# Kernel tuning notes

Measured on AMD Instinct MI355X. Metric: run time of the kernel, lower is better.

Reference implementation:

```python
import jax, jax.numpy as jnp
import numpy as np

B_SZ, L, D = 8, 8192, 256


def setup_inputs() -> dict:
    key = jax.random.key(0)
    kx, ka, kb, kc = jax.random.split(key, 4)
    x = jax.random.normal(kx, (B_SZ, L, D), dtype=jnp.float32)
    # Scale A so its spectral radius is < 1; otherwise the 8192-step linear
    # recurrence overflows. (Random Gaussian DxD with std s has norm ~ 2*s*sqrt(D).)
    A = jax.random.normal(ka, (D, D), dtype=jnp.float32) * (0.4 / np.sqrt(D))
    B = jax.random.normal(kb, (D, D), dtype=jnp.float32) * 0.05
    C = jax.random.normal(kc, (D, D), dtype=jnp.float32) * 0.05
    return {"x": x, "A": A, "B": B, "C": C}


def reference(x, A, B, C):
    # state_t = state_{t-1} @ A + x_t @ B.T ; out_t = state_t @ C.T
    # Dropout is identity in eval mode and omitted.
    b = x.shape[0]
    h = A.shape[0]
    init = jnp.zeros((b, h), dtype=x.dtype)
    Bt = B.T  # (input_dim, hidden_dim) -> math uses x @ B.T per source
    Ct = C.T

    def step(state, xt):  # xt: (b, d)
        state = state @ A + xt @ Bt
        return state, state @ Ct

    _, ys = jax.lax.scan(step, init, jnp.swapaxes(x, 0, 1))  # ys: (l, b, out)
    return jnp.swapaxes(ys, 0, 1)  # (b, l, out)
```

## Files before the change

kernel.cpp:

```cpp
#include <hip/hip_runtime.h>

#define BSZ 8
#define LSEQ 8192
#define DDIM 256
#define CHUNK 16
#define WARM 32
#define STEPS (CHUNK + WARM)
#define CPB 16

typedef float f32x4 __attribute__((ext_vector_type(4)));
typedef _Float16 h8 __attribute__((ext_vector_type(8)));
typedef _Float16 h4 __attribute__((ext_vector_type(4)));
typedef _Float16 h2 __attribute__((ext_vector_type(2)));


__global__ __launch_bounds__(256) void k_gemm_u(
    const float* __restrict__ x, const float* __restrict__ A,
    const float* __restrict__ B, const float* __restrict__ C,
    _Float16* __restrict__ U, _Float16* __restrict__ AhT,
    _Float16* __restrict__ Ch, _Float16* __restrict__ Zph) {
  __shared__ __align__(16) _Float16 xh[64][264];
  __shared__ __align__(16) _Float16 bs[64][264];
  const int tid = threadIdx.x, wv = tid >> 6, lane = tid & 63;
  const int l15 = lane & 15, q = lane >> 4;

  if (blockIdx.x < 256) {
    const int r = blockIdx.x;
    AhT[tid * 256 + r] = (_Float16)A[r * 256 + tid];
    Ch[r * 256 + tid] = (_Float16)C[r * 256 + tid];
    if (r == 0) { Zph[tid] = (_Float16)0.f; Zph[tid + 256] = (_Float16)0.f; }
  }

  const size_t rowbase = (size_t)blockIdx.x * 64;
#pragma unroll 4
  for (int i = 0; i < 16; ++i) {
    const int f4 = i * 256 + tid;
    const int row = f4 >> 6, c4 = f4 & 63;
    float4 v = *(const float4*)(x + (rowbase + row) * 256 + c4 * 4);
    h4 h;
    h[0] = (_Float16)v.x; h[1] = (_Float16)v.y; h[2] = (_Float16)v.z; h[3] = (_Float16)v.w;
    *(h4*)&xh[row][c4 * 4] = h;
  }

#pragma unroll 1
  for (int cbk = 0; cbk < 4; ++cbk) {
    __syncthreads();
#pragma unroll 4
    for (int i = 0; i < 16; ++i) {
      const int f4 = i * 256 + tid;
      const int row = f4 >> 6, c4 = f4 & 63;
      float4 v = *(const float4*)(B + (size_t)(cbk * 64 + row) * 256 + c4 * 4);
      h4 h;
      h[0] = (_Float16)v.x; h[1] = (_Float16)v.y; h[2] = (_Float16)v.z; h[3] = (_Float16)v.w;
      *(h4*)&bs[row][c4 * 4] = h;
    }
    __syncthreads();

    f32x4 acc[4] = {};
#pragma unroll
    for (int kb = 0; kb < 8; ++kb) {
      h8 af = *(const h8*)&xh[wv * 16 + l15][kb * 32 + q * 8];
#pragma unroll
      for (int ct = 0; ct < 4; ++ct) {
        h8 bf = *(const h8*)&bs[ct * 16 + l15][kb * 32 + q * 8];
        acc[ct] = __builtin_amdgcn_mfma_f32_16x16x32_f16(af, bf, acc[ct], 0, 0, 0);
      }
    }
    const size_t grow = rowbase + wv * 16 + q * 4;
#pragma unroll
    for (int r = 0; r < 4; ++r) {
      h4 hv;
      hv[0] = (_Float16)acc[0][r]; hv[1] = (_Float16)acc[1][r];
      hv[2] = (_Float16)acc[2][r]; hv[3] = (_Float16)acc[3][r];
      *(h4*)(U + (grow + r) * 256 + cbk * 64 + l15 * 4) = hv;
    }
  }
}

__global__ __launch_bounds__(512, 2) void k_scan(const _Float16* __restrict__ U,
                                                 const _Float16* __restrict__ AhT,
                                                 const _Float16* __restrict__ Ch,
                                                 const _Float16* __restrict__ Zp,
                                                 float* __restrict__ O) {
  __shared__ __align__(16) _Float16 st[2][CPB][264];
  const int tid = threadIdx.x, wv = tid >> 6, lane = tid & 63;
  const int l15 = lane & 15, q = lane >> 4;
  const int g64 = wv >> 1, hf = wv & 1;
  const int b = blockIdx.x >> 5;
  const int c0 = (blockIdx.x & 31) * CPB;
  const size_t bbase = (size_t)b * LSEQ;

  h8 bf[2][8], cf[2][8];
#pragma unroll
  for (int ctl = 0; ctl < 2; ++ctl)
#pragma unroll
    for (int kb = 0; kb < 8; ++kb) {
      const size_t mo = (size_t)(g64 * 64 + (2 * hf + ctl) * 16 + l15) * 256 + kb * 32 + q * 8;
      bf[ctl][kb] = *(const h8*)(AhT + mo);
      cf[ctl][kb] = *(const h8*)(Ch + mo);
    }

  for (int i = tid; i < CPB * 264; i += 512) ((_Float16*)st[0])[i] = (_Float16)0.f;

  auto uload = [&](int t, int r) -> h2 {
    const int lr = (c0 + q * 4 + r) * CHUNK + t;
    const _Float16* p = (lr < 0 || lr >= LSEQ)
                            ? (Zp + l15 * 4 + 2 * hf)
                            : (U + (bbase + (size_t)lr) * 256 + g64 * 64 + l15 * 4 + 2 * hf);
    return *(const h2*)p;
  };

  float* op[4];
#pragma unroll
  for (int r = 0; r < 4; ++r)
    op[r] = O + (bbase + (size_t)(c0 + q * 4 + r) * CHUNK) * 256 + g64 * 64 + 2 * hf * 16 + l15;

  h2 up0 = uload(-WARM, 0), up1 = uload(-WARM, 1), up2 = uload(-WARM, 2), up3 = uload(-WARM, 3);
  __syncthreads();

  int cb = 0;
#pragma unroll 1
  for (int g = 0; g <= STEPS; ++g) {
    const int t = g - WARM;
    h2 un0 = uload(t + 1, 0), un1 = uload(t + 1, 1), un2 = uload(t + 1, 2), un3 = uload(t + 1, 3);
    if (g < STEPS) {
      f32x4 acc[2];
#pragma unroll
      for (int ctl = 0; ctl < 2; ++ctl) {
        acc[ctl][0] = (float)up0[ctl]; acc[ctl][1] = (float)up1[ctl];
        acc[ctl][2] = (float)up2[ctl]; acc[ctl][3] = (float)up3[ctl];
      }
      if (t >= 1) {
        f32x4 acc2[2] = {};
#pragma unroll
        for (int kb = 0; kb < 8; ++kb) {
          h8 af = *(const h8*)&st[cb][l15][kb * 32 + q * 8];
#pragma unroll
          for (int ctl = 0; ctl < 2; ++ctl)
            acc[ctl] = __builtin_amdgcn_mfma_f32_16x16x32_f16(af, bf[ctl][kb], acc[ctl], 0, 0, 0);
#pragma unroll
          for (int ctl = 0; ctl < 2; ++ctl)
            acc2[ctl] = __builtin_amdgcn_mfma_f32_16x16x32_f16(af, cf[ctl][kb], acc2[ctl], 0, 0, 0);
        }
#pragma unroll
        for (int ctl = 0; ctl < 2; ++ctl)
#pragma unroll
          for (int r = 0; r < 4; ++r)
            st[cb ^ 1][q * 4 + r][g64 * 64 + (2 * hf + ctl) * 16 + l15] = (_Float16)acc[ctl][r];
#pragma unroll
        for (int r = 0; r < 4; ++r) {
          op[r][0] = acc2[0][r];
          op[r][16] = acc2[1][r];
          op[r] += 256;
        }
      } else {
#pragma unroll
        for (int kb = 0; kb < 8; ++kb) {
          h8 af = *(const h8*)&st[cb][l15][kb * 32 + q * 8];
#pragma unroll
          for (int ctl = 0; ctl < 2; ++ctl)
            acc[ctl] = __builtin_amdgcn_mfma_f32_16x16x32_f16(af, bf[ctl][kb], acc[ctl], 0, 0, 0);
        }
#pragma unroll
        for (int ctl = 0; ctl < 2; ++ctl)
#pragma unroll
          for (int r = 0; r < 4; ++r)
            st[cb ^ 1][q * 4 + r][g64 * 64 + (2 * hf + ctl) * 16 + l15] = (_Float16)acc[ctl][r];
      }
    } else {
      f32x4 acc2[2] = {};
#pragma unroll
      for (int kb = 0; kb < 8; ++kb) {
        h8 af = *(const h8*)&st[cb][l15][kb * 32 + q * 8];
#pragma unroll
        for (int ctl = 0; ctl < 2; ++ctl)
          acc2[ctl] = __builtin_amdgcn_mfma_f32_16x16x32_f16(af, cf[ctl][kb], acc2[ctl], 0, 0, 0);
      }
#pragma unroll
      for (int r = 0; r < 4; ++r) {
        op[r][0] = acc2[0][r];
        op[r][16] = acc2[1][r];
      }
    }
    asm volatile("s_waitcnt lgkmcnt(0)" ::: "memory");
    __builtin_amdgcn_s_barrier();
    asm volatile("" ::: "memory");
    up0 = un0; up1 = un1; up2 = un2; up3 = un3;
    cb ^= 1;
  }
}

extern "C" void kernel_launch(void* const* d_in, const int* in_sizes, int n_in,
                              void* d_out, int out_size, void* d_ws, size_t ws_size,
                              hipStream_t stream) {
  const float* x = (const float*)d_in[0];
  const float* A = (const float*)d_in[1];
  const float* B = (const float*)d_in[2];
  const float* C = (const float*)d_in[3];

  char* ws = (char*)d_ws;
  _Float16* U = (_Float16*)ws;
  _Float16* AhT = (_Float16*)(ws + 33554432);
  _Float16* Ch = (_Float16*)(ws + 33554432 + 131072);
  _Float16* Zph = (_Float16*)(ws + 33554432 + 262144);
  float* out = (float*)d_out;

  hipLaunchKernelGGL(k_gemm_u, dim3(1024), dim3(256), 0, stream, x, A, B, C, U, AhT,
                     Ch, Zph);
  hipLaunchKernelGGL(k_scan, dim3(256), dim3(512), 0, stream, U, AhT, Ch, Zph, out);
}
```

Baseline: 178.0 us.

## Load B fragments directly into registers and halve rows per GEMM block

The U = x·Bᵀ GEMM kernel no longer stages B through shared memory in four column chunks with barriers. Each wave now reads its 64 output columns of B straight from global memory into registers, converting to fp16 on the way, and reuses them across two 16-row tiles. Blocks cover 32 rows instead of 64 and the grid doubles, which cuts LDS use and barriers. The cost is that every block rereads all of B from global or L2 memory, and there is less reuse per block.

```diff
diff --git a/kernel.cpp b/kernel.cpp
--- a/kernel.cpp
+++ b/kernel.cpp
@@ -19,8 +19,7 @@
     const float* __restrict__ B, const float* __restrict__ C,
     _Float16* __restrict__ U, _Float16* __restrict__ AhT,
     _Float16* __restrict__ Ch, _Float16* __restrict__ Zph) {
-  __shared__ __align__(16) _Float16 xh[64][264];
-  __shared__ __align__(16) _Float16 bs[64][264];
+  __shared__ __align__(16) _Float16 xh[32][264];
   const int tid = threadIdx.x, wv = tid >> 6, lane = tid & 63;
   const int l15 = lane & 15, q = lane >> 4;
 
@@ -31,9 +30,9 @@
     if (r == 0) { Zph[tid] = (_Float16)0.f; Zph[tid + 256] = (_Float16)0.f; }
   }
 
-  const size_t rowbase = (size_t)blockIdx.x * 64;
-#pragma unroll 4
-  for (int i = 0; i < 16; ++i) {
+  const size_t rowbase = (size_t)blockIdx.x * 32;
+#pragma unroll
+  for (int i = 0; i < 8; ++i) {
     const int f4 = i * 256 + tid;
     const int row = f4 >> 6, c4 = f4 & 63;
     float4 v = *(const float4*)(x + (rowbase + row) * 256 + c4 * 4);
@@ -41,38 +40,39 @@
     h[0] = (_Float16)v.x; h[1] = (_Float16)v.y; h[2] = (_Float16)v.z; h[3] = (_Float16)v.w;
     *(h4*)&xh[row][c4 * 4] = h;
   }
-
-#pragma unroll 1
-  for (int cbk = 0; cbk < 4; ++cbk) {
-    __syncthreads();
-#pragma unroll 4
-    for (int i = 0; i < 16; ++i) {
-      const int f4 = i * 256 + tid;
-      const int row = f4 >> 6, c4 = f4 & 63;
-      float4 v = *(const float4*)(B + (size_t)(cbk * 64 + row) * 256 + c4 * 4);
-      h4 h;
-      h[0] = (_Float16)v.x; h[1] = (_Float16)v.y; h[2] = (_Float16)v.z; h[3] = (_Float16)v.w;
-      *(h4*)&bs[row][c4 * 4] = h;
-    }
-    __syncthreads();
-
-    f32x4 acc[4] = {};
+  __syncthreads();
+
+  f32x4 acc[2][4] = {};
+#pragma unroll
+  for (int ct = 0; ct < 4; ++ct) {
+    const int n = wv * 64 + ct * 16 + l15;
+    h8 bf[8];
 #pragma unroll
     for (int kb = 0; kb < 8; ++kb) {
-      h8 af = *(const h8*)&xh[wv * 16 + l15][kb * 32 + q * 8];
-#pragma unroll
-      for (int ct = 0; ct < 4; ++ct) {
-        h8 bf = *(const h8*)&bs[ct * 16 + l15][kb * 32 + q * 8];
-        acc[ct] = __builtin_amdgcn_mfma_f32_16x16x32_f16(af, bf, acc[ct], 0, 0, 0);
-      }
-    }
-    const size_t grow = rowbase + wv * 16 + q * 4;
+      const float* bp = B + (size_t)n * 256 + kb * 32 + q * 8;
+      float4 b0 = *(const float4*)bp, b1 = *(const float4*)(bp + 4);
+      h8 f;
+      f[0] = (_Float16)b0.x; f[1] = (_Float16)b0.y; f[2] = (_Float16)b0.z; f[3] = (_Float16)b0.w;
+      f[4] = (_Float16)b1.x; f[5] = (_Float16)b1.y; f[6] = (_Float16)b1.z; f[7] = (_Float16)b1.w;
+      bf[kb] = f;
+    }
+#pragma unroll
+    for (int rt = 0; rt < 2; ++rt)
+#pragma unroll
+      for (int kb = 0; kb < 8; ++kb) {
+        h8 af = *(const h8*)&xh[rt * 16 + l15][kb * 32 + q * 8];
+        acc[rt][ct] = __builtin_amdgcn_mfma_f32_16x16x32_f16(af, bf[kb], acc[rt][ct], 0, 0, 0);
+      }
+  }
+#pragma unroll
+  for (int rt = 0; rt < 2; ++rt) {
+    const size_t grow = rowbase + rt * 16 + q * 4;
 #pragma unroll
     for (int r = 0; r < 4; ++r) {
       h4 hv;
-      hv[0] = (_Float16)acc[0][r]; hv[1] = (_Float16)acc[1][r];
-      hv[2] = (_Float16)acc[2][r]; hv[3] = (_Float16)acc[3][r];
-      *(h4*)(U + (grow + r) * 256 + cbk * 64 + l15 * 4) = hv;
+      hv[0] = (_Float16)acc[rt][0][r]; hv[1] = (_Float16)acc[rt][1][r];
+      hv[2] = (_Float16)acc[rt][2][r]; hv[3] = (_Float16)acc[rt][3][r];
+      *(h4*)(U + (grow + r) * 256 + wv * 64 + l15 * 4) = hv;
     }
   }
 }
@@ -205,7 +205,7 @@
   _Float16* Zph = (_Float16*)(ws + 33554432 + 262144);
   float* out = (float*)d_out;
 
-  hipLaunchKernelGGL(k_gemm_u, dim3(1024), dim3(256), 0, stream, x, A, B, C, U, AhT,
+  hipLaunchKernelGGL(k_gemm_u, dim3(2048), dim3(256), 0, stream, x, A, B, C, U, AhT,
                      Ch, Zph);
   hipLaunchKernelGGL(k_scan, dim3(256), dim3(512), 0, stream, U, AhT, Ch, Zph, out);
 }
```

Measured after the change: 206.7 us. +16.1%, slower.
